# Performance work log

Hardware: AMD Instinct MI355X
Metric: run time of the kernel (lower is better)

The kernel has to match this reference:

```python
import jax, jax.numpy as jnp
import numpy as np

B, N, F, NCG, NCONV, VOCAB = 16, 1024, 128, 64, 3, 100
EPS = 0.001


def setup_inputs() -> dict:
    key = jax.random.key(0)
    ks = jax.random.split(key, 16)
    atoms_nodes = jax.random.randint(ks[0], (B, N), 0, VOCAB, dtype=jnp.int32)
    xyz = jax.random.normal(ks[1], (B, N, 3), jnp.float32) * 3.0
    # chain bonds (i, i+1) per molecule -> every atom has degree >= 1
    bi = jnp.repeat(jnp.arange(B), N - 1)
    si = jnp.tile(jnp.arange(N - 1), B)
    bonds = jnp.stack([bi, si, si + 1], axis=1).astype(jnp.int32)  # [B*(N-1), 3]
    tau = jnp.float32(1.0)
    gumbel_u = jax.random.uniform(ks[2], (B, N, NCG), jnp.float32, 1e-6, 1.0 - 1e-6)
    # parameters
    emb = jax.random.normal(ks[3], (VOCAB, F), jnp.float32) * 0.1
    emb = emb.at[0].set(0.0)  # padding_idx=0
    s = 1.0 / np.sqrt(F)
    upd_W1 = jax.random.uniform(ks[4], (NCONV, F, F), jnp.float32, -s, s)
    upd_b1 = jax.random.uniform(ks[5], (NCONV, F), jnp.float32, -s, s)
    upd_W2 = jax.random.uniform(ks[6], (NCONV, F, F), jnp.float32, -s, s)
    upd_b2 = jax.random.uniform(ks[7], (NCONV, F), jnp.float32, -s, s)
    cg_W1 = jax.random.uniform(ks[8], (F, F), jnp.float32, -s, s)
    cg_b1 = jax.random.uniform(ks[9], (F,), jnp.float32, -s, s)
    cg_W2 = jax.random.uniform(ks[10], (F, NCG), jnp.float32, -s, s)
    cg_b2 = jax.random.uniform(ks[11], (NCG,), jnp.float32, -s, s)
    return {"atoms_nodes": atoms_nodes, "xyz": xyz, "bonds": bonds, "tau": tau,
            "gumbel_u": gumbel_u, "emb": emb,
            "upd_W1": upd_W1, "upd_b1": upd_b1, "upd_W2": upd_W2, "upd_b2": upd_b2,
            "cg_W1": cg_W1, "cg_b1": cg_b1, "cg_W2": cg_W2, "cg_b2": cg_b2}


def reference(atoms_nodes, xyz, bonds, tau, gumbel_u, emb,
              upd_W1, upd_b1, upd_W2, upd_b2, cg_W1, cg_b1, cg_W2, cg_b2):
    h = emb[atoms_nodes]  # [B,N,F]
    # dense symmetric adjacency from bond list
    adj = jnp.zeros((B, N, N), jnp.float32)
    adj = adj.at[bonds[:, 0], bonds[:, 1], bonds[:, 2]].set(1.0)
    adj = adj.at[bonds[:, 0], bonds[:, 2], bonds[:, 1]].set(1.0)
    deg = jnp.sum(adj, axis=-1)[:, :, None]  # [B,N,1]
    for l in range(NCONV):
        ch = jnp.tanh(h @ upd_W1[l] + upd_b1[l]) @ upd_W2[l] + upd_b2[l]
        dh = jnp.einsum('bif,bij->bjf', ch, adj) / deg
        h = h + dh
    # gumbel-softmax assignment (soft)
    assign_logits = jnp.tanh(h @ cg_W1 + cg_b1) @ cg_W2 + cg_b2  # [B,N,NCG]
    g = -jnp.log(-jnp.log(gumbel_u))
    M = jax.nn.softmax((assign_logits + g) / tau, axis=-1)  # [B,N,NCG]
    M_norm = M / jnp.sum(M, axis=-2, keepdims=True)
    H = jnp.einsum('bnj,bnf->bjf', M_norm, h)        # [B,NCG,F]
    cg_xyz = jnp.einsum('bin,bij->bjn', xyz, M_norm)  # [B,NCG,3]
    cg_adj = jnp.broadcast_to(jnp.ones((NCG, NCG)) - jnp.eye(NCG), (B, NCG, NCG))
    diff = cg_xyz[:, :, None, :] - cg_xyz[:, None, :, :]
    dist = jnp.sqrt(jnp.sum(diff * diff, axis=-1) + EPS)  # [B,NCG,NCG]
    knbrs = jnp.argsort(dist, axis=-1)
    return (M, M_norm, h, H, adj, cg_xyz, cg_adj, knbrs)
```

## Files before the change

### kernel.cpp

```cpp
#include <hip/hip_runtime.h>
#include <math.h>

#define BB 16
#define NN 1024
#define FF 128
#define NCG 64
#define NCONV 3
#define CAP 8

static const size_t O_M     = 0;
static const size_t O_MN    = (size_t)BB*NN*NCG;
static const size_t O_H     = O_MN  + (size_t)BB*NN*NCG;
static const size_t O_HH    = O_H   + (size_t)BB*NN*FF;
static const size_t O_ADJ   = O_HH  + (size_t)BB*NCG*FF;
static const size_t O_CGXYZ = O_ADJ + (size_t)BB*NN*NN;
static const size_t O_CGADJ = O_CGXYZ + (size_t)BB*NCG*3;
static const size_t O_KN    = O_CGADJ + (size_t)BB*NCG*NCG;

static const size_t S_H64  = 0;
static const size_t S_CH64 = (size_t)BB*NN*FF;
static const size_t S_LM64 = S_CH64 + (size_t)BB*NN*FF;
static const size_t S_HPF  = 5242880;
static const size_t S_CGP  = 5767168;
static const size_t S_NBR  = 6291456;
static const size_t S_W64  = 6553600;

static const size_t WO_CONV = 0;
static const size_t WO_CGW1 = 98304;
static const size_t WO_CGW2 = 114688;
static const int    W64_N   = 122880;

static const size_t W_INVD = 0;
static const size_t W_COLS = (size_t)BB*NN;
static const size_t W_CG64 = W_COLS + (size_t)BB*NCG;
static const size_t W_CNT  = W_CG64 + (size_t)BB*NCG*3;

__global__ void k_zero(int* cnt) {
    int i = blockIdx.x * blockDim.x + threadIdx.x;
    if (i < BB*NN) cnt[i] = 0;
}

__global__ void k_build_nbr(const int* __restrict__ bonds, int nb, int* cnt, int* nbr) {
    int i = blockIdx.x * blockDim.x + threadIdx.x;
    if (i >= nb) return;
    int b = bonds[i*3+0], s = bonds[i*3+1], t = bonds[i*3+2];
    int ns = b*NN + s, nt = b*NN + t;
    int p = atomicAdd(&cnt[ns], 1);
    if (p < CAP) nbr[(size_t)ns*CAP + p] = nt;
    int q = atomicAdd(&cnt[nt], 1);
    if (q < CAP) nbr[(size_t)nt*CAP + q] = ns;
}

__global__ void k_invdeg(const int* __restrict__ cnt, double* invdeg) {
    int i = blockIdx.x * blockDim.x + threadIdx.x;
    if (i >= BB*NN) return;
    int d = cnt[i];
    invdeg[i] = d > 0 ? 1.0 / (double)d : 0.0;
}

__global__ void k_cgadj(float* cgadj) {
    int idx = blockIdx.x * blockDim.x + threadIdx.x;
    if (idx >= BB*NCG*NCG) return;
    int i = (idx / NCG) % NCG, j = idx % NCG;
    cgadj[idx] = (i == j) ? 0.f : 1.f;
}

__global__ void k_emb64(const int* __restrict__ atoms, const float* __restrict__ emb,
                        double* __restrict__ h) {
    int idx = blockIdx.x * blockDim.x + threadIdx.x;
    if (idx >= BB*NN*(FF/4)) return;
    int n = idx / (FF/4), f4 = idx % (FF/4);
    int a = atoms[n];
    const float4 v = *reinterpret_cast<const float4*>(&emb[(size_t)a*FF + f4*4]);
    double* hp = &h[(size_t)n*FF + f4*4];
    hp[0] = (double)v.x; hp[1] = (double)v.y; hp[2] = (double)v.z; hp[3] = (double)v.w;
}

__global__ void k_cvtW(const float* __restrict__ uW1, const float* __restrict__ uW2,
                       const float* __restrict__ cgW1, const float* __restrict__ cgW2,
                       double* __restrict__ W64) {
    int idx = blockIdx.x * blockDim.x + threadIdx.x;
    if (idx >= W64_N) return;
    float v;
    if (idx < 98304) {
        int l = idx >> 15, r = idx & 32767;
        v = (r < 16384) ? uW1[l*16384 + r] : uW2[l*16384 + (r & 16383)];
    } else if (idx < 114688) {
        v = cgW1[idx - 98304];
    } else {
        v = cgW2[idx - 114688];
    }
    W64[idx] = (double)v;
}

template<int COUT2>
__global__ __launch_bounds__(256) void k_layer(const double* __restrict__ in,
        const double* __restrict__ W1, const float* __restrict__ b1,
        const double* __restrict__ W2, const float* __restrict__ b2,
        double* __restrict__ out) {
    constexpr int K = 128, KC = 32;
    constexpr int ASTR = 34, TSTR = 130;
    constexpr int NW2 = KC*COUT2/2/256;
    __shared__ double As[32*ASTR];
    __shared__ double ts[32*TSTR];
    __shared__ double Ws[KC*128];
    const int tid = threadIdx.x;
    const size_t row0 = (size_t)blockIdx.x * 32;
    const double2* in2  = reinterpret_cast<const double2*>(in + row0*K);
    const double2* W1_2 = reinterpret_cast<const double2*>(W1);
    const double2* W2_2 = reinterpret_cast<const double2*>(W2);
    double2* Ws2 = reinterpret_cast<double2*>(Ws);

    const int tc = tid & 15, tr = tid >> 4;
    const int r0 = tr * 2;

    double acc[2][8];
    #pragma unroll
    for (int i = 0; i < 2; ++i)
        #pragma unroll
        for (int j = 0; j < 8; ++j) acc[i][j] = 0.0;

    double2 pA[2], pW[8];
    #pragma unroll
    for (int i = 0; i < 2; ++i) { int q = tid + i*256; pA[i] = in2[(q>>4)*64 + (q&15)]; }
    #pragma unroll
    for (int i = 0; i < 8; ++i) pW[i] = W1_2[tid + i*256];

    for (int kc = 0; kc < K; kc += KC) {
        __syncthreads();
        #pragma unroll
        for (int i = 0; i < 2; ++i) {
            int q = tid + i*256;
            *reinterpret_cast<double2*>(&As[(q>>4)*ASTR + (q&15)*2]) = pA[i];
        }
        #pragma unroll
        for (int i = 0; i < 8; ++i) Ws2[tid + i*256] = pW[i];
        if (kc + KC < K) {
            const int kn = kc + KC;
            #pragma unroll
            for (int i = 0; i < 2; ++i) { int q = tid + i*256; pA[i] = in2[(q>>4)*64 + (kn>>1) + (q&15)]; }
            #pragma unroll
            for (int i = 0; i < 8; ++i) pW[i] = W1_2[kn*64 + tid + i*256];
        }
        __syncthreads();
        #pragma unroll
        for (int kk2 = 0; kk2 < KC/2; ++kk2) {
            double2 a0 = *reinterpret_cast<const double2*>(&As[(r0+0)*ASTR + kk2*2]);
            double2 a1 = *reinterpret_cast<const double2*>(&As[(r0+1)*ASTR + kk2*2]);
            const double2* w0 = reinterpret_cast<const double2*>(&Ws[(kk2*2+0)*128]);
            const double2* w1 = reinterpret_cast<const double2*>(&Ws[(kk2*2+1)*128]);
            #pragma unroll
            for (int g = 0; g < 4; ++g) {
                double2 u0 = w0[tc + g*16];
                double2 u1 = w1[tc + g*16];
                acc[0][g*2+0] += a0.x*u0.x; acc[0][g*2+1] += a0.x*u0.y;
                acc[1][g*2+0] += a1.x*u0.x; acc[1][g*2+1] += a1.x*u0.y;
                acc[0][g*2+0] += a0.y*u1.x; acc[0][g*2+1] += a0.y*u1.y;
                acc[1][g*2+0] += a1.y*u1.x; acc[1][g*2+1] += a1.y*u1.y;
            }
        }
    }
    #pragma unroll
    for (int g = 0; g < 4; ++g) {
        int c = tc*2 + g*32;
        double bb0 = (double)b1[c], bb1 = (double)b1[c+1];
        #pragma unroll
        for (int i = 0; i < 2; ++i) {
            double2 o;
            o.x = tanh(acc[i][g*2+0] + bb0);
            o.y = tanh(acc[i][g*2+1] + bb1);
            *reinterpret_cast<double2*>(&ts[(r0+i)*TSTR + c]) = o;
        }
    }

    constexpr int CT2  = COUT2/8;
    constexpr int RPT2 = (COUT2 == 128) ? 2 : 1;
    const int tc2 = tid % CT2, tr2 = tid / CT2;
    const int rB = tr2 * RPT2;
    double acc2[RPT2][8];
    #pragma unroll
    for (int i = 0; i < RPT2; ++i)
        #pragma unroll
        for (int j = 0; j < 8; ++j) acc2[i][j] = 0.0;

    #pragma unroll
    for (int i = 0; i < NW2; ++i) pW[i] = W2_2[tid + i*256];

    for (int kc = 0; kc < K; kc += KC) {
        __syncthreads();
        #pragma unroll
        for (int i = 0; i < NW2; ++i) Ws2[tid + i*256] = pW[i];
        if (kc + KC < K) {
            const int kn = kc + KC;
            #pragma unroll
            for (int i = 0; i < NW2; ++i) pW[i] = W2_2[kn*(COUT2/2) + tid + i*256];
        }
        __syncthreads();
        #pragma unroll
        for (int kk2 = 0; kk2 < KC/2; ++kk2) {
            double2 a[RPT2];
            #pragma unroll
            for (int i = 0; i < RPT2; ++i)
                a[i] = *reinterpret_cast<const double2*>(&ts[(rB+i)*TSTR + kc + kk2*2]);
            const double2* w0 = reinterpret_cast<const double2*>(&Ws[(kk2*2+0)*COUT2]);
            const double2* w1 = reinterpret_cast<const double2*>(&Ws[(kk2*2+1)*COUT2]);
            #pragma unroll
            for (int g = 0; g < 4; ++g) {
                double2 u0 = w0[tc2 + g*CT2];
                double2 u1 = w1[tc2 + g*CT2];
                #pragma unroll
                for (int i = 0; i < RPT2; ++i) {
                    acc2[i][g*2+0] += a[i].x*u0.x; acc2[i][g*2+1] += a[i].x*u0.y;
                    acc2[i][g*2+0] += a[i].y*u1.x; acc2[i][g*2+1] += a[i].y*u1.y;
                }
            }
        }
    }
    #pragma unroll
    for (int g = 0; g < 4; ++g) {
        int c = tc2*2 + g*(COUT2/4);
        double bb0 = (double)b2[c], bb1 = (double)b2[c+1];
        #pragma unroll
        for (int i = 0; i < RPT2; ++i) {
            double2 o;
            o.x = acc2[i][g*2+0] + bb0;
            o.y = acc2[i][g*2+1] + bb1;
            *reinterpret_cast<double2*>(&out[(row0 + rB + i)*COUT2 + c]) = o;
        }
    }
}

template<bool WRITE_F32>
__global__ void k_gather(const double* __restrict__ ch, const double* __restrict__ invdeg,
                         const int* __restrict__ nbr, const int* __restrict__ cnt,
                         double* __restrict__ h, float* __restrict__ hout) {
    int idx = blockIdx.x * blockDim.x + threadIdx.x;
    if (idx >= BB*NN*(FF/4)) return;
    int node = idx >> 5, f4 = idx & 31;
    int c = cnt[node];
    double2 s0; s0.x = 0.0; s0.y = 0.0;
    double2 s1 = s0;
    for (int q = 0; q < c; ++q) {
        int nb = nbr[(size_t)node*CAP + q];
        const double2* cp = reinterpret_cast<const double2*>(ch + (size_t)nb*FF + f4*4);
        double2 a = cp[0], b2 = cp[1];
        s0.x += a.x; s0.y += a.y; s1.x += b2.x; s1.y += b2.y;
    }
    double w = invdeg[node];
    double2* hp = reinterpret_cast<double2*>(h + (size_t)node*FF + f4*4);
    double2 h0 = hp[0], h1 = hp[1];
    h0.x += s0.x*w; h0.y += s0.y*w; h1.x += s1.x*w; h1.y += s1.y*w;
    hp[0] = h0; hp[1] = h1;
    if (WRITE_F32) {
        float4 o; o.x = (float)h0.x; o.y = (float)h0.y; o.z = (float)h1.x; o.w = (float)h1.y;
        *reinterpret_cast<float4*>(&hout[(size_t)node*FF + f4*4]) = o;
    }
}

__global__ void k_softmax64(double* __restrict__ lm, const float* __restrict__ gum,
                            const float* __restrict__ tau_p, float* __restrict__ M_out) {
    int row = blockIdx.x * 4 + threadIdx.x / 64;
    int lane = threadIdx.x & 63;
    double tau = (double)(*tau_p);
    double u = (double)gum[(size_t)row*NCG + lane];
    double g = -log(-log(u));
    double v = (lm[(size_t)row*NCG + lane] + g) / tau;
    double m = v;
    #pragma unroll
    for (int off = 32; off; off >>= 1) m = fmax(m, __shfl_xor(m, off));
    double e = exp(v - m);
    double s = e;
    #pragma unroll
    for (int off = 32; off; off >>= 1) s += __shfl_xor(s, off);
    double mv = e / s;
    lm[(size_t)row*NCG + lane] = mv;
    M_out[(size_t)row*NCG + lane] = (float)mv;
}

__global__ __launch_bounds__(256) void k_cols(const double* __restrict__ M,
                                              double* __restrict__ colsum) {
    __shared__ double red[256];
    int b = blockIdx.x;
    int tid = threadIdx.x;
    int j = tid & 63, q = tid >> 6;
    const double* Mb = M + (size_t)b*NN*NCG;
    double s = 0.0;
    for (int n = q*256; n < q*256 + 256; ++n) s += Mb[(size_t)n*NCG + j];
    red[tid] = s;
    __syncthreads();
    if (tid < 64) {
        colsum[b*NCG + j] = red[j] + red[64+j] + red[128+j] + red[192+j];
    }
}

__global__ void k_mnorm_out(const double* __restrict__ M, const double* __restrict__ colsum,
                            float* __restrict__ Mn) {
    size_t i = (size_t)blockIdx.x * blockDim.x + threadIdx.x;
    if (i >= (size_t)BB*NN*NCG) return;
    size_t b = i >> 16;
    int j = (int)(i & 63);
    Mn[i] = (float)(M[i] / colsum[b*NCG + j]);
}

__global__ __launch_bounds__(256) void k_Hpart32(const float* __restrict__ Mn,
                                                 const float* __restrict__ h,
                                                 float* __restrict__ Hp) {
    __shared__ float Ms[32*NCG];
    __shared__ float hs[32*FF];
    const int b = blockIdx.x, ch = blockIdx.y;
    const int tid = threadIdx.x;
    const int tc = tid % 32, tr = tid / 32;
    const float4* M4 = reinterpret_cast<const float4*>(Mn + (size_t)b*NN*NCG);
    const float4* h4 = reinterpret_cast<const float4*>(h + (size_t)b*NN*FF);
    float4* Ms4 = reinterpret_cast<float4*>(Ms);
    float4* hs4 = reinterpret_cast<float4*>(hs);
    const float2* Ms2 = reinterpret_cast<const float2*>(Ms);
    const float2* hs2 = reinterpret_cast<const float2*>(hs);

    float acc[8][4];
    #pragma unroll
    for (int i = 0; i < 8; ++i)
        #pragma unroll
        for (int j = 0; j < 4; ++j) acc[i][j] = 0.f;

    for (int s = 0; s < 4; ++s) {
        const int n0 = ch*128 + s*32;
        __syncthreads();
        #pragma unroll
        for (int i = 0; i < 2; ++i) Ms4[tid + i*256] = M4[n0*16 + tid + i*256];
        #pragma unroll
        for (int i = 0; i < 4; ++i) hs4[tid + i*256] = h4[n0*32 + tid + i*256];
        __syncthreads();
        for (int n = 0; n < 32; ++n) {
            float2 hv0 = hs2[n*64 + tc];
            float2 hv1 = hs2[n*64 + 32 + tc];
            float2 m0 = Ms2[n*32 + tr];
            float2 m1 = Ms2[n*32 + 8 + tr];
            float2 m2 = Ms2[n*32 + 16 + tr];
            float2 m3 = Ms2[n*32 + 24 + tr];
            float mj[8] = {m0.x, m0.y, m1.x, m1.y, m2.x, m2.y, m3.x, m3.y};
            #pragma unroll
            for (int jj = 0; jj < 8; ++jj) {
                acc[jj][0] += mj[jj]*hv0.x; acc[jj][1] += mj[jj]*hv0.y;
                acc[jj][2] += mj[jj]*hv1.x; acc[jj][3] += mj[jj]*hv1.y;
            }
        }
    }
    float* Ho = Hp + ((size_t)ch*BB + b) * NCG * FF;
    #pragma unroll
    for (int gj = 0; gj < 4; ++gj)
        #pragma unroll
        for (int pj = 0; pj < 2; ++pj) {
            int j = tr*2 + gj*16 + pj;
            int jj = gj*2 + pj;
            float2 o0; o0.x = acc[jj][0]; o0.y = acc[jj][1];
            float2 o1; o1.x = acc[jj][2]; o1.y = acc[jj][3];
            float2* op = reinterpret_cast<float2*>(Ho + (size_t)j*FF);
            op[tc] = o0; op[32 + tc] = o1;
        }
}

__global__ void k_Hfin32(const float* __restrict__ Hp, float* __restrict__ H) {
    int idx = blockIdx.x * blockDim.x + threadIdx.x;
    if (idx >= BB*NCG*FF) return;
    int b = idx / (NCG*FF);
    int r = idx % (NCG*FF);
    float s = 0.f;
    #pragma unroll
    for (int c = 0; c < 8; ++c) s += Hp[((size_t)c*BB + b)*NCG*FF + r];
    H[idx] = s;
}

__global__ __launch_bounds__(192) void k_cgpart(const double* __restrict__ M,
                                                const float* __restrict__ xyz,
                                                double* __restrict__ cgp) {
    __shared__ double Ms[32*NCG];
    __shared__ double xs[32*3];
    const int b = blockIdx.x, ch = blockIdx.y;
    const int tid = threadIdx.x;
    const int j = tid / 3, d = tid % 3;
    const double2* M2 = reinterpret_cast<const double2*>(M + (size_t)b*NN*NCG);
    double2* Ms2 = reinterpret_cast<double2*>(Ms);
    const float* xb = xyz + (size_t)b*NN*3;
    double acc = 0.0;
    for (int s = 0; s < 4; ++s) {
        const int n0 = ch*128 + s*32;
        __syncthreads();
        for (int q = tid; q < 1024; q += 192) Ms2[q] = M2[n0*32 + q];
        for (int q = tid; q < 96; q += 192) xs[q] = (double)xb[n0*3 + q];
        __syncthreads();
        for (int n = 0; n < 32; ++n)
            acc += Ms[n*NCG + j] * xs[n*3 + d];
    }
    cgp[((size_t)ch*BB + b)*NCG*3 + tid] = acc;
}

__global__ void k_cgfin(const double* __restrict__ cgp, const double* __restrict__ colsum,
                        double* __restrict__ cg64, float* __restrict__ cg) {
    int idx = blockIdx.x * blockDim.x + threadIdx.x;
    if (idx >= BB*NCG*3) return;
    int b = idx / (NCG*3);
    int r = idx % (NCG*3);
    int j = r / 3;
    double s = 0.0;
    #pragma unroll
    for (int c = 0; c < 8; ++c) s += cgp[((size_t)c*BB + b)*NCG*3 + r];
    double v = s / colsum[b*NCG + j];
    cg64[idx] = v;
    cg[idx] = (float)v;
}

__global__ __launch_bounds__(1024) void k_knbrs(const double* __restrict__ cg,
                                                float* __restrict__ kn) {
    __shared__ double cs[NCG*3];
    const int b = blockIdx.x;
    const int tid = threadIdx.x;
    const int i = blockIdx.y * 16 + tid / 64;
    const int j = tid & 63;
    if (tid < NCG*3) cs[tid] = cg[(size_t)b*NCG*3 + tid];
    __syncthreads();
    double xi = cs[i*3+0], yi = cs[i*3+1], zi = cs[i*3+2];
    double dxj = xi - cs[j*3+0], dyj = yi - cs[j*3+1], dzj = zi - cs[j*3+2];
    double d2j = dxj*dxj + dyj*dyj + dzj*dzj;
    int rank = 0;
    for (int k = 0; k < NCG; ++k) {
        double dx = xi - cs[k*3+0], dy = yi - cs[k*3+1], dz = zi - cs[k*3+2];
        double d2k = dx*dx + dy*dy + dz*dz;
        rank += (d2k < d2j) || (d2k == d2j && k < j);
    }
    kn[(size_t)b*NCG*NCG + (size_t)i*NCG + rank] = (float)j;
}

__global__ void k_zero_adj(float4* adj4, long n4) {
    long i = (long)blockIdx.x * blockDim.x + threadIdx.x;
    long stride = (long)gridDim.x * blockDim.x;
    float4 z; z.x = z.y = z.z = z.w = 0.f;
    for (; i < n4; i += stride) adj4[i] = z;
}

__global__ void k_bonds_adj(const int* __restrict__ bonds, int nb, float* adj) {
    int i = blockIdx.x * blockDim.x + threadIdx.x;
    if (i >= nb) return;
    int b = bonds[i*3+0], s = bonds[i*3+1], t = bonds[i*3+2];
    size_t base = (size_t)b * NN * NN;
    adj[base + (size_t)s*NN + t] = 1.f;
    adj[base + (size_t)t*NN + s] = 1.f;
}

extern "C" void kernel_launch(void* const* d_in, const int* in_sizes, int n_in,
                              void* d_out, int out_size, void* d_ws, size_t ws_size,
                              hipStream_t stream) {
    const int*   atoms  = (const int*)  d_in[0];
    const float* xyz    = (const float*)d_in[1];
    const int*   bonds  = (const int*)  d_in[2];
    const float* tau    = (const float*)d_in[3];
    const float* gum    = (const float*)d_in[4];
    const float* emb    = (const float*)d_in[5];
    const float* uW1    = (const float*)d_in[6];
    const float* ub1    = (const float*)d_in[7];
    const float* uW2    = (const float*)d_in[8];
    const float* ub2    = (const float*)d_in[9];
    const float* cgW1   = (const float*)d_in[10];
    const float* cgb1   = (const float*)d_in[11];
    const float* cgW2   = (const float*)d_in[12];
    const float* cgb2   = (const float*)d_in[13];

    float* out = (float*)d_out;
    float* o_M   = out + O_M;
    float* o_Mn  = out + O_MN;
    float* o_h   = out + O_H;
    float* o_H   = out + O_HH;
    float* o_adj = out + O_ADJ;
    float* o_cg  = out + O_CGXYZ;
    float* o_ca  = out + O_CGADJ;
    float* o_kn  = out + O_KN;

    double* scr  = (double*)o_adj;
    double* h64  = scr + S_H64;
    double* ch64 = scr + S_CH64;
    double* lm64 = scr + S_LM64;
    float*  Hpf  = (float*)(scr + S_HPF);
    double* cgp  = scr + S_CGP;
    int*    nbr  = (int*)(scr + S_NBR);
    double* W64  = scr + S_W64;

    double* wsd    = (double*)d_ws;
    double* invdeg = wsd + W_INVD;
    double* colsum = wsd + W_COLS;
    double* cg64   = wsd + W_CG64;
    int*    cnt    = (int*)(wsd + W_CNT);

    const int nb = in_sizes[2] / 3;

    hipLaunchKernelGGL(k_zero, dim3(64), dim3(256), 0, stream, cnt);
    hipLaunchKernelGGL(k_build_nbr, dim3((nb+255)/256), dim3(256), 0, stream,
                       bonds, nb, cnt, nbr);
    hipLaunchKernelGGL(k_invdeg, dim3(64), dim3(256), 0, stream, cnt, invdeg);
    hipLaunchKernelGGL(k_cgadj, dim3(256), dim3(256), 0, stream, o_ca);
    hipLaunchKernelGGL(k_cvtW, dim3((W64_N+255)/256), dim3(256), 0, stream,
                       uW1, uW2, cgW1, cgW2, W64);
    hipLaunchKernelGGL(k_emb64, dim3(2048), dim3(256), 0, stream, atoms, emb, h64);

    for (int l = 0; l < NCONV; ++l) {
        hipLaunchKernelGGL((k_layer<128>), dim3(512), dim3(256), 0, stream,
                           h64, W64 + (size_t)l*32768, ub1 + (size_t)l*FF,
                           W64 + (size_t)l*32768 + 16384, ub2 + (size_t)l*FF, ch64);
        if (l < NCONV-1)
            hipLaunchKernelGGL((k_gather<false>), dim3(2048), dim3(256), 0, stream,
                               ch64, invdeg, nbr, cnt, h64, o_h);
        else
            hipLaunchKernelGGL((k_gather<true>), dim3(2048), dim3(256), 0, stream,
                               ch64, invdeg, nbr, cnt, h64, o_h);
    }

    hipLaunchKernelGGL((k_layer<64>), dim3(512), dim3(256), 0, stream,
                       h64, W64 + WO_CGW1, cgb1, W64 + WO_CGW2, cgb2, lm64);

    hipLaunchKernelGGL(k_softmax64, dim3(4096), dim3(256), 0, stream,
                       lm64, gum, tau, o_M);
    hipLaunchKernelGGL(k_cols, dim3(16), dim3(256), 0, stream, lm64, colsum);
    hipLaunchKernelGGL(k_mnorm_out, dim3(4096), dim3(256), 0, stream, lm64, colsum, o_Mn);
    hipLaunchKernelGGL(k_Hpart32, dim3(BB, 8), dim3(256), 0, stream, o_Mn, o_h, Hpf);
    hipLaunchKernelGGL(k_Hfin32, dim3(512), dim3(256), 0, stream, Hpf, o_H);
    hipLaunchKernelGGL(k_cgpart, dim3(BB, 8), dim3(192), 0, stream, lm64, xyz, cgp);
    hipLaunchKernelGGL(k_cgfin, dim3(12), dim3(256), 0, stream, cgp, colsum, cg64, o_cg);
    hipLaunchKernelGGL(k_knbrs, dim3(BB, 4), dim3(1024), 0, stream, cg64, o_kn);

    hipLaunchKernelGGL(k_zero_adj, dim3(4096), dim3(256), 0, stream,
                       (float4*)o_adj, (long)BB*NN*NN/4);
    hipLaunchKernelGGL(k_bonds_adj, dim3((nb+255)/256), dim3(256), 0, stream,
                       bonds, nb, o_adj);
}
```

Baseline: 419.8 us.

## Split fused two-GEMM MLP layer into separate generic fp64 GEMM kernels

```diff
diff --git a/kernel.cpp b/kernel.cpp
--- a/kernel.cpp
+++ b/kernel.cpp
@@ -18,14 +18,13 @@
 static const size_t O_KN    = O_CGADJ + (size_t)BB*NCG*NCG;
 
 static const size_t S_H64  = 0;
-static const size_t S_CH64 = (size_t)BB*NN*FF;
-static const size_t S_LM64 = S_CH64 + (size_t)BB*NN*FF;
+static const size_t S_T64  = (size_t)BB*NN*FF;
+static const size_t S_LM64 = S_T64 + (size_t)BB*NN*FF;
 static const size_t S_HPF  = 5242880;
 static const size_t S_CGP  = 5767168;
 static const size_t S_NBR  = 6291456;
 static const size_t S_W64  = 6553600;
 
-static const size_t WO_CONV = 0;
 static const size_t WO_CGW1 = 98304;
 static const size_t WO_CGW2 = 114688;
 static const int    W64_N   = 122880;
@@ -93,139 +92,79 @@
     W64[idx] = (double)v;
 }
 
-template<int COUT2>
-__global__ __launch_bounds__(256) void k_layer(const double* __restrict__ in,
-        const double* __restrict__ W1, const float* __restrict__ b1,
-        const double* __restrict__ W2, const float* __restrict__ b2,
-        double* __restrict__ out) {
-    constexpr int K = 128, KC = 32;
-    constexpr int ASTR = 34, TSTR = 130;
-    constexpr int NW2 = KC*COUT2/2/256;
-    __shared__ double As[32*ASTR];
-    __shared__ double ts[32*TSTR];
-    __shared__ double Ws[KC*128];
+template<int COUT, bool TANH>
+__global__ __launch_bounds__(256) void k_gemm64(const double* __restrict__ in,
+                                                const double* __restrict__ W,
+                                                const float* __restrict__ bias,
+                                                double* __restrict__ out) {
+    constexpr int K = 128, ROWS = 32, KC = 32;
+    constexpr int ASTR = K + 2;
+    constexpr int NW = KC*COUT/512;
+    constexpr int CT = COUT/8;
+    constexpr int RPT = ROWS*CT/256;
+    __shared__ double As[ROWS*ASTR];
+    __shared__ double Ws[KC*COUT];
     const int tid = threadIdx.x;
-    const size_t row0 = (size_t)blockIdx.x * 32;
-    const double2* in2  = reinterpret_cast<const double2*>(in + row0*K);
-    const double2* W1_2 = reinterpret_cast<const double2*>(W1);
-    const double2* W2_2 = reinterpret_cast<const double2*>(W2);
+    const size_t row0 = (size_t)blockIdx.x * ROWS;
+    const double2* in2 = reinterpret_cast<const double2*>(in + row0*K);
+    const double2* Wg  = reinterpret_cast<const double2*>(W);
     double2* Ws2 = reinterpret_cast<double2*>(Ws);
 
-    const int tc = tid & 15, tr = tid >> 4;
-    const int r0 = tr * 2;
-
-    double acc[2][8];
-    #pragma unroll
-    for (int i = 0; i < 2; ++i)
+    #pragma unroll
+    for (int i = 0; i < 8; ++i) {
+        int q = tid + i*256;
+        *reinterpret_cast<double2*>(&As[(q>>6)*ASTR + (q&63)*2]) = in2[q];
+    }
+    double2 pW[NW];
+    #pragma unroll
+    for (int i = 0; i < NW; ++i) pW[i] = Wg[tid + i*256];
+
+    const int tc = tid % CT, tr = tid / CT;
+    const int r0 = tr * RPT;
+    double acc[RPT][8];
+    #pragma unroll
+    for (int i = 0; i < RPT; ++i)
         #pragma unroll
         for (int j = 0; j < 8; ++j) acc[i][j] = 0.0;
 
-    double2 pA[2], pW[8];
-    #pragma unroll
-    for (int i = 0; i < 2; ++i) { int q = tid + i*256; pA[i] = in2[(q>>4)*64 + (q&15)]; }
-    #pragma unroll
-    for (int i = 0; i < 8; ++i) pW[i] = W1_2[tid + i*256];
-
     for (int kc = 0; kc < K; kc += KC) {
         __syncthreads();
         #pragma unroll
-        for (int i = 0; i < 2; ++i) {
-            int q = tid + i*256;
-            *reinterpret_cast<double2*>(&As[(q>>4)*ASTR + (q&15)*2]) = pA[i];
+        for (int i = 0; i < NW; ++i) Ws2[tid + i*256] = pW[i];
+        if (kc + KC < K) {
+            #pragma unroll
+            for (int i = 0; i < NW; ++i) pW[i] = Wg[(kc+KC)*(COUT/2) + tid + i*256];
         }
-        #pragma unroll
-        for (int i = 0; i < 8; ++i) Ws2[tid + i*256] = pW[i];
-        if (kc + KC < K) {
-            const int kn = kc + KC;
+        __syncthreads();
+        #pragma unroll
+        for (int kk = 0; kk < KC; ++kk) {
+            double a[RPT];
             #pragma unroll
-            for (int i = 0; i < 2; ++i) { int q = tid + i*256; pA[i] = in2[(q>>4)*64 + (kn>>1) + (q&15)]; }
-            #pragma unroll
-            for (int i = 0; i < 8; ++i) pW[i] = W1_2[kn*64 + tid + i*256];
-        }
-        __syncthreads();
-        #pragma unroll
-        for (int kk2 = 0; kk2 < KC/2; ++kk2) {
-            double2 a0 = *reinterpret_cast<const double2*>(&As[(r0+0)*ASTR + kk2*2]);
-            double2 a1 = *reinterpret_cast<const double2*>(&As[(r0+1)*ASTR + kk2*2]);
-            const double2* w0 = reinterpret_cast<const double2*>(&Ws[(kk2*2+0)*128]);
-            const double2* w1 = reinterpret_cast<const double2*>(&Ws[(kk2*2+1)*128]);
+            for (int i = 0; i < RPT; ++i) a[i] = As[(r0+i)*ASTR + kc + kk];
+            const double2* wrow = reinterpret_cast<const double2*>(&Ws[kk*COUT]);
             #pragma unroll
             for (int g = 0; g < 4; ++g) {
-                double2 u0 = w0[tc + g*16];
-                double2 u1 = w1[tc + g*16];
-                acc[0][g*2+0] += a0.x*u0.x; acc[0][g*2+1] += a0.x*u0.y;
-                acc[1][g*2+0] += a1.x*u0.x; acc[1][g*2+1] += a1.x*u0.y;
-                acc[0][g*2+0] += a0.y*u1.x; acc[0][g*2+1] += a0.y*u1.y;
-                acc[1][g*2+0] += a1.y*u1.x; acc[1][g*2+1] += a1.y*u1.y;
-            }
-        }
-    }
-    #pragma unroll
-    for (int g = 0; g < 4; ++g) {
-        int c = tc*2 + g*32;
-        double bb0 = (double)b1[c], bb1 = (double)b1[c+1];
-        #pragma unroll
-        for (int i = 0; i < 2; ++i) {
-            double2 o;
-            o.x = tanh(acc[i][g*2+0] + bb0);
-            o.y = tanh(acc[i][g*2+1] + bb1);
-            *reinterpret_cast<double2*>(&ts[(r0+i)*TSTR + c]) = o;
-        }
-    }
-
-    constexpr int CT2  = COUT2/8;
-    constexpr int RPT2 = (COUT2 == 128) ? 2 : 1;
-    const int tc2 = tid % CT2, tr2 = tid / CT2;
-    const int rB = tr2 * RPT2;
-    double acc2[RPT2][8];
-    #pragma unroll
-    for (int i = 0; i < RPT2; ++i)
-        #pragma unroll
-        for (int j = 0; j < 8; ++j) acc2[i][j] = 0.0;
-
-    #pragma unroll
-    for (int i = 0; i < NW2; ++i) pW[i] = W2_2[tid + i*256];
-
-    for (int kc = 0; kc < K; kc += KC) {
-        __syncthreads();
-        #pragma unroll
-        for (int i = 0; i < NW2; ++i) Ws2[tid + i*256] = pW[i];
-        if (kc + KC < K) {
-            const int kn = kc + KC;
-            #pragma unroll
-            for (int i = 0; i < NW2; ++i) pW[i] = W2_2[kn*(COUT2/2) + tid + i*256];
-        }
-        __syncthreads();
-        #pragma unroll
-        for (int kk2 = 0; kk2 < KC/2; ++kk2) {
-            double2 a[RPT2];
-            #pragma unroll
-            for (int i = 0; i < RPT2; ++i)
-                a[i] = *reinterpret_cast<const double2*>(&ts[(rB+i)*TSTR + kc + kk2*2]);
-            const double2* w0 = reinterpret_cast<const double2*>(&Ws[(kk2*2+0)*COUT2]);
-            const double2* w1 = reinterpret_cast<const double2*>(&Ws[(kk2*2+1)*COUT2]);
-            #pragma unroll
-            for (int g = 0; g < 4; ++g) {
-                double2 u0 = w0[tc2 + g*CT2];
-                double2 u1 = w1[tc2 + g*CT2];
+                double2 u = wrow[tc + g*CT];
                 #pragma unroll
-                for (int i = 0; i < RPT2; ++i) {
-                    acc2[i][g*2+0] += a[i].x*u0.x; acc2[i][g*2+1] += a[i].x*u0.y;
-                    acc2[i][g*2+0] += a[i].y*u1.x; acc2[i][g*2+1] += a[i].y*u1.y;
+                for (int i = 0; i < RPT; ++i) {
+                    acc[i][g*2+0] += a[i]*u.x;
+                    acc[i][g*2+1] += a[i]*u.y;
                 }
             }
         }
     }
+
     #pragma unroll
     for (int g = 0; g < 4; ++g) {
-        int c = tc2*2 + g*(COUT2/4);
-        double bb0 = (double)b2[c], bb1 = (double)b2[c+1];
-        #pragma unroll
-        for (int i = 0; i < RPT2; ++i) {
+        int c = tc*2 + g*(COUT/4);
+        double b0 = (double)bias[c], b1 = (double)bias[c+1];
+        #pragma unroll
+        for (int i = 0; i < RPT; ++i) {
             double2 o;
-            o.x = acc2[i][g*2+0] + bb0;
-            o.y = acc2[i][g*2+1] + bb1;
-            *reinterpret_cast<double2*>(&out[(row0 + rB + i)*COUT2 + c]) = o;
+            o.x = acc[i][g*2+0] + b0;
+            o.y = acc[i][g*2+1] + b1;
+            if (TANH) { o.x = tanh(o.x); o.y = tanh(o.y); }
+            *reinterpret_cast<double2*>(&out[(row0 + r0 + i)*COUT + c]) = o;
         }
     }
 }
@@ -477,7 +416,7 @@
 
     double* scr  = (double*)o_adj;
     double* h64  = scr + S_H64;
-    double* ch64 = scr + S_CH64;
+    double* t64  = scr + S_T64;
     double* lm64 = scr + S_LM64;
     float*  Hpf  = (float*)(scr + S_HPF);
     double* cgp  = scr + S_CGP;
@@ -502,19 +441,22 @@
     hipLaunchKernelGGL(k_emb64, dim3(2048), dim3(256), 0, stream, atoms, emb, h64);
 
     for (int l = 0; l < NCONV; ++l) {
-        hipLaunchKernelGGL((k_layer<128>), dim3(512), dim3(256), 0, stream,
-                           h64, W64 + (size_t)l*32768, ub1 + (size_t)l*FF,
-                           W64 + (size_t)l*32768 + 16384, ub2 + (size_t)l*FF, ch64);
+        hipLaunchKernelGGL((k_gemm64<128,true>), dim3(512), dim3(256), 0, stream,
+                           h64, W64 + (size_t)l*32768, ub1 + (size_t)l*FF, t64);
+        hipLaunchKernelGGL((k_gemm64<128,false>), dim3(512), dim3(256), 0, stream,
+                           t64, W64 + (size_t)l*32768 + 16384, ub2 + (size_t)l*FF, t64);
         if (l < NCONV-1)
             hipLaunchKernelGGL((k_gather<false>), dim3(2048), dim3(256), 0, stream,
-                               ch64, invdeg, nbr, cnt, h64, o_h);
+                               t64, invdeg, nbr, cnt, h64, o_h);
         else
             hipLaunchKernelGGL((k_gather<true>), dim3(2048), dim3(256), 0, stream,
-                               ch64, invdeg, nbr, cnt, h64, o_h);
-    }
-
-    hipLaunchKernelGGL((k_layer<64>), dim3(512), dim3(256), 0, stream,
-                       h64, W64 + WO_CGW1, cgb1, W64 + WO_CGW2, cgb2, lm64);
+                               t64, invdeg, nbr, cnt, h64, o_h);
+    }
+
+    hipLaunchKernelGGL((k_gemm64<128,true>), dim3(512), dim3(256), 0, stream,
+                       h64, W64 + WO_CGW1, cgb1, t64);
+    hipLaunchKernelGGL((k_gemm64<64,false>), dim3(512), dim3(256), 0, stream,
+                       t64, W64 + WO_CGW2, cgb2, lm64);
 
     hipLaunchKernelGGL(k_softmax64, dim3(4096), dim3(256), 0, stream,
                        lm64, gum, tau, o_M);
```

Measured after the change: 451.0 us. 7.4% more time.
